# Kernel tuning notes

Measured on AMD Instinct MI355X. Metric: run time of the kernel, lower is better.

The kernel has to match this reference:

```python
import jax, jax.numpy as jnp
import numpy as np

WINDOW_SIZE = 11
SIGMA = 1.5
C1 = 0.01 ** 2
C2 = 0.03 ** 2


def _gaussian_window(channel, dtype):
    # 1D gaussian, normalized, then outer product -> 2D window, expanded per channel
    xs = np.arange(WINDOW_SIZE) - WINDOW_SIZE // 2
    g = np.exp(-(xs.astype(np.float64) ** 2) / (2.0 * SIGMA ** 2))
    g = (g / g.sum()).astype(np.float32)
    w2d = np.outer(g, g)  # [ws, ws]
    w = np.broadcast_to(w2d[None, None], (channel, 1, WINDOW_SIZE, WINDOW_SIZE))
    return jnp.asarray(w, dtype=dtype)


def _depthwise_conv(img, window, channel):
    pad = WINDOW_SIZE // 2
    return jax.lax.conv_general_dilated(
        img, window,
        window_strides=(1, 1),
        padding=[(pad, pad), (pad, pad)],
        dimension_numbers=('NCHW', 'OIHW', 'NCHW'),
        feature_group_count=channel)


def setup_inputs() -> dict:
    key = jax.random.key(0)
    k1, k2 = jax.random.split(key)
    shape = (16, 3, 512, 512)
    x = jax.random.uniform(k1, shape, dtype=jnp.float32)
    y = jax.random.uniform(k2, shape, dtype=jnp.float32)
    return {"x": x, "y": y}


def reference(x, y):
    channel = x.shape[-3]
    window = _gaussian_window(channel, x.dtype)

    mu1 = _depthwise_conv(x, window, channel)
    mu2 = _depthwise_conv(y, window, channel)
    mu1_sq = mu1 * mu1
    mu2_sq = mu2 * mu2
    mu1_mu2 = mu1 * mu2
    sigma1_sq = _depthwise_conv(x * x, window, channel) - mu1_sq
    sigma2_sq = _depthwise_conv(y * y, window, channel) - mu2_sq
    sigma12 = _depthwise_conv(x * y, window, channel) - mu1_mu2

    ssim_map = ((2.0 * mu1_mu2 + C1) * (2.0 * sigma12 + C2)) / (
        (mu1_sq + mu2_sq + C1) * (sigma1_sq + sigma2_sq + C2))
    # DSSIM = 1 - mean(ssim)
    return 1.0 - jnp.mean(ssim_map)
```

## Files before the change

kernel.cpp:

```cpp
#include <hip/hip_runtime.h>


typedef _Float16 half8 __attribute__((ext_vector_type(8)));
typedef _Float16 half4v __attribute__((ext_vector_type(4)));
typedef __fp16 pk16 __attribute__((ext_vector_type(2)));
typedef float f32x4 __attribute__((ext_vector_type(4)));
typedef float f32x8 __attribute__((ext_vector_type(8)));

#define IMG_W   512
#define IMG_H   512
#define NPLANES 48
#define BR      16
#define TP      40
#define GRX     (IMG_H / BR)
#define NBLK    (GRX * NPLANES)

__device__ __forceinline__ unsigned pkrtz_u(float a, float b) {
    union { pk16 p; unsigned u; } c;
    c.p = __builtin_amdgcn_cvt_pkrtz(a, b);
    return c.u;
}

__global__ __launch_bounds__(256, 3)
void dssim_main(const float* __restrict__ xin, const float* __restrict__ yin,
                float* __restrict__ partial) {
    __shared__ _Float16 ldsT[4][4][16][TP];
    __shared__ float wpart[4];

    const int t    = threadIdx.x;
    const int lane = t & 63;
    const int wid  = t >> 6;
    const int bn   = lane & 15;
    const int jg   = lane >> 4;
    const int swz  = (bn & 8) << 1;
    const int r0   = blockIdx.x * BR;
    const size_t pbase = (size_t)blockIdx.y * (IMG_W * IMG_H);
    const float* __restrict__ xp = xin + pbase;
    const float* __restrict__ yp = yin + pbase;

    float ginv;
    {
        float s = 0.f;
#pragma unroll
        for (int i = 0; i < 11; ++i) {
            float d = (float)(i - 5);
            s += expf(-(d * d) * (1.0f / 4.5f));
        }
        ginv = 1.0f / s;
    }

    half8 whF, wvF;
#pragma unroll
    for (int j = 0; j < 8; ++j) {
        const int k = 8 * jg + j;
        const int dh = k - bn - 3;
        const int dv = k - bn;
        float wh = 0.f, wv = 0.f;
        if (dh >= 0 && dh < 11) {
            const float d = (float)(dh - 5);
            wh = ginv * expf(-(d * d) * (1.0f / 4.5f));
        }
        if (dv >= 0 && dv < 11) {
            const float d = (float)(dv - 5);
            wv = ginv * expf(-(d * d) * (1.0f / 4.5f));
        }
        whF[j] = (_Float16)wh;
        wvF[j] = (_Float16)wv;
    }

    const int gr0 = r0 - 5 + bn;
    const bool rowok0 = (gr0 >= 0) && (gr0 < IMG_H);
    const int gr1 = r0 + 11 + bn;
    const bool rowok1 = (bn < 10) && (gr1 < IMG_H);
    const size_t row0 = (size_t)(rowok0 ? gr0 : 0) * IMG_W;
    const size_t row1 = (size_t)(rowok1 ? gr1 : 0) * IMG_W;

    const f32x8 z8 = {0.f, 0.f, 0.f, 0.f, 0.f, 0.f, 0.f, 0.f};
    const f32x4 zf = {0.f, 0.f, 0.f, 0.f};
    const float C1 = 0.0001f, C2 = 0.0009f;
    float lsum = 0.f;

    f32x8 xs0, ys0, xs1, ys1;

#define LOADI(ii)                                                           \
    {                                                                       \
        const int col = (((wid + 4 * (ii)) << 4) + 8 * jg) - 8;             \
        const bool colok = (col >= 0) && (col < IMG_W);                     \
        const size_t co = (size_t)(colok ? col : 0);                        \
        const bool ok0 = colok && rowok0, ok1 = colok && rowok1;            \
        xs0 = ok0 ? *(const f32x8*)(xp + row0 + co) : z8;                   \
        ys0 = ok0 ? *(const f32x8*)(yp + row0 + co) : z8;                   \
        xs1 = ok1 ? *(const f32x8*)(xp + row1 + co) : z8;                   \
        ys1 = ok1 ? *(const f32x8*)(yp + row1 + co) : z8;                   \
    }

#define HCOMPI(ii)                                                          \
    {                                                                       \
        _Pragma("unroll")                                                   \
        for (int rt = 0; rt < 2; ++rt) {                                    \
            const f32x8 xv = rt ? xs1 : xs0;                                \
            const f32x8 yv = rt ? ys1 : ys0;                                \
            const f32x8 su = xv + yv;                                       \
            const f32x8 sw = xv - yv;                                       \
            union { unsigned u[4]; half8 h; } aU, aW;                       \
            _Pragma("unroll")                                               \
            for (int d = 0; d < 4; ++d) {                                   \
                aU.u[d] = pkrtz_u(su[2 * d], su[2 * d + 1]);                \
                aW.u[d] = pkrtz_u(sw[2 * d], sw[2 * d + 1]);                \
            }                                                               \
            const half8 aU2 = aU.h * aU.h;                                  \
            const half8 aW2 = aW.h * aW.h;                                  \
            const f32x4 cU  = __builtin_amdgcn_mfma_f32_16x16x32_f16(aU.h, whF, zf, 0, 0, 0); \
            const f32x4 cW  = __builtin_amdgcn_mfma_f32_16x16x32_f16(aW.h, whF, zf, 0, 0, 0); \
            const f32x4 cU2 = __builtin_amdgcn_mfma_f32_16x16x32_f16(aU2,  whF, zf, 0, 0, 0); \
            const f32x4 cW2 = __builtin_amdgcn_mfma_f32_16x16x32_f16(aW2,  whF, zf, 0, 0, 0); \
            union { unsigned u[2]; half4v h; } hU, hW, hU2, hW2;            \
            _Pragma("unroll")                                               \
            for (int q = 0; q < 2; ++q) {                                   \
                hU.u[q]  = pkrtz_u(cU[2 * q],  cU[2 * q + 1]);              \
                hW.u[q]  = pkrtz_u(cW[2 * q],  cW[2 * q + 1]);              \
                hU2.u[q] = pkrtz_u(cU2[2 * q], cU2[2 * q + 1]);             \
                hW2.u[q] = pkrtz_u(cW2[2 * q], cW2[2 * q + 1]);             \
            }                                                               \
            const int kk = (16 * rt + 4 * jg) ^ swz;                        \
            *(half4v*)&ldsT[wid][0][bn][kk] = hU.h;                         \
            *(half4v*)&ldsT[wid][1][bn][kk] = hW.h;                         \
            *(half4v*)&ldsT[wid][2][bn][kk] = hU2.h;                        \
            *(half4v*)&ldsT[wid][3][bn][kk] = hW2.h;                        \
        }                                                                   \
    }

#define VBLURI(ii)                                                          \
    {                                                                       \
        const int kb = (8 * jg) ^ swz;                                      \
        const half8 aTU  = *(const half8*)&ldsT[wid][0][bn][kb];            \
        const half8 aTW  = *(const half8*)&ldsT[wid][1][bn][kb];            \
        const half8 aTU2 = *(const half8*)&ldsT[wid][2][bn][kb];            \
        const half8 aTW2 = *(const half8*)&ldsT[wid][3][bn][kb];            \
        const f32x4 accU = __builtin_amdgcn_mfma_f32_16x16x32_f16(aTU,  wvF, zf, 0, 0, 0); \
        const f32x4 accW = __builtin_amdgcn_mfma_f32_16x16x32_f16(aTW,  wvF, zf, 0, 0, 0); \
        const f32x4 accP = __builtin_amdgcn_mfma_f32_16x16x32_f16(aTU2, wvF, zf, 0, 0, 0); \
        const f32x4 accQ = __builtin_amdgcn_mfma_f32_16x16x32_f16(aTW2, wvF, zf, 0, 0, 0); \
        _Pragma("unroll")                                                   \
        for (int q = 0; q < 4; ++q) {                                       \
            const float U = accU[q], W = accW[q];                           \
            const float P = accP[q], Q = accQ[q];                           \
            const float U2 = U * U, W2 = W * W;                             \
            const float A = 0.5f * (U2 + W2);                               \
            const float B = 0.5f * (U2 - W2);                               \
            const float den2 = fmaf(0.5f, P + Q, -A) + C2;                  \
            const float num2 = fmaf(0.5f, P - Q, -B) + C2;                  \
            lsum += (B + C1) * num2 * __builtin_amdgcn_rcpf((A + C1) * den2); \
        }                                                                   \
    }

    LOADI(0);
    HCOMPI(0);
#pragma unroll
    for (int i = 0; i < 8; ++i) {
        if (i + 1 < 8) LOADI(i + 1);
        VBLURI(i);
        if (i + 1 < 8) HCOMPI(i + 1);
    }

#pragma unroll
    for (int off = 32; off >= 1; off >>= 1)
        lsum += __shfl_down(lsum, off, 64);
    if (lane == 0) wpart[wid] = lsum;
    __syncthreads();
    if (t == 0) {
        partial[(size_t)blockIdx.y * GRX + blockIdx.x] =
            wpart[0] + wpart[1] + wpart[2] + wpart[3];
    }
}

__global__ __launch_bounds__(256)
void dssim_final(const float* __restrict__ partial, float* __restrict__ out) {
    __shared__ double wsum[4];
    double s = 0.0;
    for (int i = threadIdx.x; i < NBLK; i += 256) s += (double)partial[i];
#pragma unroll
    for (int off = 32; off >= 1; off >>= 1)
        s += __shfl_down(s, off, 64);
    if ((threadIdx.x & 63) == 0) wsum[threadIdx.x >> 6] = s;
    __syncthreads();
    if (threadIdx.x == 0) {
        const double tot = wsum[0] + wsum[1] + wsum[2] + wsum[3];
        out[0] = (float)(1.0 - tot / 12582912.0);
    }
}

extern "C" void kernel_launch(void* const* d_in, const int* in_sizes, int n_in,
                              void* d_out, int out_size, void* d_ws, size_t ws_size,
                              hipStream_t stream) {
    const float* x = (const float*)d_in[0];
    const float* y = (const float*)d_in[1];
    float* out = (float*)d_out;
    float* partial = (float*)d_ws;

    dim3 grid(GRX, NPLANES);
    dim3 block(256);
    dssim_main<<<grid, block, 0, stream>>>(x, y, partial);
    dssim_final<<<1, block, 0, stream>>>(partial, out);
}
```

Measured before the change: 48.83 us.

## Process 32 output rows per block to amortize vertical halo loads

Doubles the row strip per block from 16 to 32 rows. Each thread now loads three input row groups instead of two and runs three horizontal MFMA passes plus two vertical blur passes per column tile. This amortizes the 10-row vertical halo over more output rows, cutting redundant global loads and horizontal work, and halves the number of blocks. In exchange it raises register pressure and LDS use per block, and the fixed grid leaves fewer blocks to fill the GPU.

Result: slower. 78.72 us (+61.2%).

```diff
diff --git a/kernel.cpp b/kernel.cpp
--- a/kernel.cpp
+++ b/kernel.cpp
@@ -10,8 +10,8 @@
 #define IMG_W   512
 #define IMG_H   512
 #define NPLANES 48
-#define BR      16
-#define TP      40
+#define BR      32
+#define TP      72
 #define GRX     (IMG_H / BR)
 #define NBLK    (GRX * NPLANES)
 
@@ -69,37 +69,41 @@
     }
 
     const int gr0 = r0 - 5 + bn;
-    const bool rowok0 = (gr0 >= 0) && (gr0 < IMG_H);
+    const bool rowok0 = (gr0 >= 0);
     const int gr1 = r0 + 11 + bn;
-    const bool rowok1 = (bn < 10) && (gr1 < IMG_H);
+    const int gr2 = r0 + 27 + bn;
+    const bool rowok2 = (bn < 10) && (gr2 < IMG_H);
     const size_t row0 = (size_t)(rowok0 ? gr0 : 0) * IMG_W;
-    const size_t row1 = (size_t)(rowok1 ? gr1 : 0) * IMG_W;
+    const size_t row1 = (size_t)gr1 * IMG_W;
+    const size_t row2 = (size_t)(rowok2 ? gr2 : 0) * IMG_W;
 
     const f32x8 z8 = {0.f, 0.f, 0.f, 0.f, 0.f, 0.f, 0.f, 0.f};
     const f32x4 zf = {0.f, 0.f, 0.f, 0.f};
     const float C1 = 0.0001f, C2 = 0.0009f;
     float lsum = 0.f;
 
-    f32x8 xs0, ys0, xs1, ys1;
+    f32x8 xs0, ys0, xs1, ys1, xs2, ys2;
 
 #define LOADI(ii)                                                           \
     {                                                                       \
         const int col = (((wid + 4 * (ii)) << 4) + 8 * jg) - 8;             \
         const bool colok = (col >= 0) && (col < IMG_W);                     \
         const size_t co = (size_t)(colok ? col : 0);                        \
-        const bool ok0 = colok && rowok0, ok1 = colok && rowok1;            \
-        xs0 = ok0 ? *(const f32x8*)(xp + row0 + co) : z8;                   \
-        ys0 = ok0 ? *(const f32x8*)(yp + row0 + co) : z8;                   \
-        xs1 = ok1 ? *(const f32x8*)(xp + row1 + co) : z8;                   \
-        ys1 = ok1 ? *(const f32x8*)(yp + row1 + co) : z8;                   \
-    }
-
-#define HCOMPI(ii)                                                          \
+        const bool ok0 = colok && rowok0, ok2 = colok && rowok2;            \
+        xs0 = ok0   ? *(const f32x8*)(xp + row0 + co) : z8;                 \
+        ys0 = ok0   ? *(const f32x8*)(yp + row0 + co) : z8;                 \
+        xs1 = colok ? *(const f32x8*)(xp + row1 + co) : z8;                 \
+        ys1 = colok ? *(const f32x8*)(yp + row1 + co) : z8;                 \
+        xs2 = ok2   ? *(const f32x8*)(xp + row2 + co) : z8;                 \
+        ys2 = ok2   ? *(const f32x8*)(yp + row2 + co) : z8;                 \
+    }
+
+#define HCOMPI()                                                            \
     {                                                                       \
         _Pragma("unroll")                                                   \
-        for (int rt = 0; rt < 2; ++rt) {                                    \
-            const f32x8 xv = rt ? xs1 : xs0;                                \
-            const f32x8 yv = rt ? ys1 : ys0;                                \
+        for (int rt = 0; rt < 3; ++rt) {                                    \
+            const f32x8 xv = (rt == 0) ? xs0 : (rt == 1) ? xs1 : xs2;       \
+            const f32x8 yv = (rt == 0) ? ys0 : (rt == 1) ? ys1 : ys2;       \
             const f32x8 su = xv + yv;                                       \
             const f32x8 sw = xv - yv;                                       \
             union { unsigned u[4]; half8 h; } aU, aW;                       \
@@ -130,37 +134,40 @@
         }                                                                   \
     }
 
-#define VBLURI(ii)                                                          \
+#define VBLURI()                                                            \
     {                                                                       \
-        const int kb = (8 * jg) ^ swz;                                      \
-        const half8 aTU  = *(const half8*)&ldsT[wid][0][bn][kb];            \
-        const half8 aTW  = *(const half8*)&ldsT[wid][1][bn][kb];            \
-        const half8 aTU2 = *(const half8*)&ldsT[wid][2][bn][kb];            \
-        const half8 aTW2 = *(const half8*)&ldsT[wid][3][bn][kb];            \
-        const f32x4 accU = __builtin_amdgcn_mfma_f32_16x16x32_f16(aTU,  wvF, zf, 0, 0, 0); \
-        const f32x4 accW = __builtin_amdgcn_mfma_f32_16x16x32_f16(aTW,  wvF, zf, 0, 0, 0); \
-        const f32x4 accP = __builtin_amdgcn_mfma_f32_16x16x32_f16(aTU2, wvF, zf, 0, 0, 0); \
-        const f32x4 accQ = __builtin_amdgcn_mfma_f32_16x16x32_f16(aTW2, wvF, zf, 0, 0, 0); \
         _Pragma("unroll")                                                   \
-        for (int q = 0; q < 4; ++q) {                                       \
-            const float U = accU[q], W = accW[q];                           \
-            const float P = accP[q], Q = accQ[q];                           \
-            const float U2 = U * U, W2 = W * W;                             \
-            const float A = 0.5f * (U2 + W2);                               \
-            const float B = 0.5f * (U2 - W2);                               \
-            const float den2 = fmaf(0.5f, P + Q, -A) + C2;                  \
-            const float num2 = fmaf(0.5f, P - Q, -B) + C2;                  \
-            lsum += (B + C1) * num2 * __builtin_amdgcn_rcpf((A + C1) * den2); \
+        for (int vb = 0; vb < 2; ++vb) {                                    \
+            const int kb = (16 * vb + 8 * jg) ^ swz;                        \
+            const half8 aTU  = *(const half8*)&ldsT[wid][0][bn][kb];        \
+            const half8 aTW  = *(const half8*)&ldsT[wid][1][bn][kb];        \
+            const half8 aTU2 = *(const half8*)&ldsT[wid][2][bn][kb];        \
+            const half8 aTW2 = *(const half8*)&ldsT[wid][3][bn][kb];        \
+            const f32x4 accU = __builtin_amdgcn_mfma_f32_16x16x32_f16(aTU,  wvF, zf, 0, 0, 0); \
+            const f32x4 accW = __builtin_amdgcn_mfma_f32_16x16x32_f16(aTW,  wvF, zf, 0, 0, 0); \
+            const f32x4 accP = __builtin_amdgcn_mfma_f32_16x16x32_f16(aTU2, wvF, zf, 0, 0, 0); \
+            const f32x4 accQ = __builtin_amdgcn_mfma_f32_16x16x32_f16(aTW2, wvF, zf, 0, 0, 0); \
+            _Pragma("unroll")                                               \
+            for (int q = 0; q < 4; ++q) {                                   \
+                const float U = accU[q], W = accW[q];                       \
+                const float P = accP[q], Q = accQ[q];                       \
+                const float U2 = U * U, W2 = W * W;                         \
+                const float A = 0.5f * (U2 + W2);                           \
+                const float B = 0.5f * (U2 - W2);                           \
+                const float den2 = fmaf(0.5f, P + Q, -A) + C2;              \
+                const float num2 = fmaf(0.5f, P - Q, -B) + C2;              \
+                lsum += (B + C1) * num2 * __builtin_amdgcn_rcpf((A + C1) * den2); \
+            }                                                               \
         }                                                                   \
     }
 
     LOADI(0);
-    HCOMPI(0);
+    HCOMPI();
 #pragma unroll
     for (int i = 0; i < 8; ++i) {
         if (i + 1 < 8) LOADI(i + 1);
-        VBLURI(i);
-        if (i + 1 < 8) HCOMPI(i + 1);
+        VBLURI();
+        if (i + 1 < 8) HCOMPI();
     }
 
 #pragma unroll
```
